# Kernel optimization log

Hardware: AMD Instinct MI355X
Metric: run time of the kernel (lower is better)

Reference implementation:

```python
import jax, jax.numpy as jnp
import numpy as np

# wav2vec2 feature-extractor conv stack config: (kernel, stride) per layer, 512 channels
CONV_CFG = [(10, 5), (3, 2), (3, 2), (3, 2), (3, 2), (2, 2), (2, 2)]
C = 512
PROJ = 256
HID = 128
NCLS = 5
N_WORDS = 64
B = 8
L = 40000


def _conv1d(h, w, stride):
    # h: [B, Cin, T], w: [Cout, Cin, K]
    return jax.lax.conv_general_dilated(
        h, w, window_strides=(stride,), padding='VALID',
        dimension_numbers=('NCH', 'OIH', 'NCH'))


def setup_inputs() -> dict:
    key = jax.random.key(0)
    ks = jax.random.split(key, 16)
    x = jax.random.normal(ks[0], (B, L), dtype=jnp.float32)
    word_ids = jax.random.randint(ks[1], (B,), 0, N_WORDS)
    convs = {}
    cin = 1
    for i, (k, s) in enumerate(CONV_CFG):
        fan = cin * k
        convs[f'conv{i}'] = jax.random.normal(ks[2 + i], (C, cin, k), dtype=jnp.float32) / np.sqrt(fan)
        cin = C
    gn_scale = jnp.ones((C,), dtype=jnp.float32)
    gn_bias = jnp.zeros((C,), dtype=jnp.float32)
    proj_w = jax.random.normal(ks[9], (PROJ, C), dtype=jnp.float32) / np.sqrt(C)
    proj_b = jnp.zeros((PROJ,), dtype=jnp.float32)
    cls_w1 = jax.random.normal(ks[10], (N_WORDS, PROJ, HID), dtype=jnp.float32) / np.sqrt(PROJ)
    cls_b1 = jnp.zeros((N_WORDS, HID), dtype=jnp.float32)
    cls_w2 = jax.random.normal(ks[11], (N_WORDS, HID, NCLS), dtype=jnp.float32) / np.sqrt(HID)
    cls_b2 = jnp.zeros((N_WORDS, NCLS), dtype=jnp.float32)
    return dict(x=x, word_ids=word_ids, gn_scale=gn_scale, gn_bias=gn_bias,
                proj_w=proj_w, proj_b=proj_b, cls_w1=cls_w1, cls_b1=cls_b1,
                cls_w2=cls_w2, cls_b2=cls_b2, **convs)


def _forward(x, convs, gn_scale, gn_bias, proj_w, proj_b, cls_w1, cls_b1, cls_w2, cls_b2, word_ids):
    h = x[:, None, :]  # [B,1,L]
    for i, (k, s) in enumerate(CONV_CFG):
        h = _conv1d(h, convs[i], s)
        if i == 0:
            # wav2vec2 group-norm: groups == channels -> per-channel norm over time
            mu = jnp.mean(h, axis=-1, keepdims=True)
            var = jnp.var(h, axis=-1, keepdims=True)
            h = (h - mu) * jax.lax.rsqrt(var + 1e-5)
            h = h * gn_scale[None, :, None] + gn_bias[None, :, None]
        h = jax.nn.gelu(h)
    feat = jnp.mean(h, axis=-1)                          # [B, 512] mean-pool over time
    feat = jax.nn.relu(feat @ proj_w.T + proj_b)         # [B, 256] (dropout = identity in eval)
    w1 = cls_w1[word_ids]                                # [B, 256, 128] routed gather
    h1 = jax.nn.relu(jnp.einsum('bd,bdh->bh', feat, w1) + cls_b1[word_ids])
    out = jnp.einsum('bh,bho->bo', h1, cls_w2[word_ids]) + cls_b2[word_ids]  # [B, 5]
    return out


def reference(x, word_ids, gn_scale, gn_bias, proj_w, proj_b, cls_w1, cls_b1, cls_w2, cls_b2,
              conv0, conv1, conv2, conv3, conv4, conv5, conv6):
    convs = [conv0, conv1, conv2, conv3, conv4, conv5, conv6]
    return _forward(x, convs, gn_scale, gn_bias, proj_w, proj_b,
                    cls_w1, cls_b1, cls_w2, cls_b2, word_ids)
```

## Files before the change

### kernel.cpp

```cpp
#include <hip/hip_runtime.h>
#include <hip/hip_bf16.h>

typedef unsigned short u16;
typedef short bf16x8 __attribute__((ext_vector_type(8)));
typedef float f32x4 __attribute__((ext_vector_type(4)));

#define CC 512

constexpr int vmimm(int n) {
    return (n & 0xF) | ((n >> 4) << 14) | (0x7 << 4) | (0xF << 8);
}

__device__ __forceinline__ float gelu_tanh(float x) {
    float x3 = x * x * x;
    float z  = 0.7978845608028654f * (x + 0.044715f * x3);
    float e  = __expf(2.0f * z);
    float th = 1.0f - 2.0f / (e + 1.0f);
    return 0.5f * x * (1.0f + th);
}

__device__ __forceinline__ u16 f2bf(float f) {
    union { float f; unsigned u; } v; v.f = f;
    unsigned r = v.u + 0x7fff + ((v.u >> 16) & 1);
    return (u16)(r >> 16);
}
__device__ __forceinline__ float bf2f(u16 h) {
    union { unsigned u; float f; } v; v.u = ((unsigned)h) << 16; return v.f;
}

__global__ __launch_bounds__(256) void conv0_stats(
    const float* __restrict__ x, const float* __restrict__ w0,
    float* __restrict__ part) {
    const int t0 = blockIdx.x * 64, b = blockIdx.y;
    __shared__ float xs[64 * 5 + 16];
    __shared__ float w0t[10 * 512];
    __shared__ float redS[4][512], redQ[4][512];
    for (int i = threadIdx.x; i < 64 * 5 + 5; i += 256) {
        int gi = t0 * 5 + i;
        xs[i] = (gi < 40000) ? x[b * 40000 + gi] : 0.0f;
    }
    for (int i = threadIdx.x; i < 5120; i += 256) {
        int c = i / 10, j = i - c * 10;
        w0t[j * 512 + c] = w0[i];
    }
    __syncthreads();
    const int lane = threadIdx.x & 63, wv = threadIdx.x >> 6;
    float wr[8][10];
#pragma unroll
    for (int q = 0; q < 8; ++q)
#pragma unroll
        for (int j = 0; j < 10; ++j) wr[q][j] = w0t[j * 512 + lane + 64 * q];
    float sacc[8] = {}, qacc[8] = {};
#pragma unroll
    for (int u = 0; u < 16; ++u) {
        const int tt = wv * 16 + u;
        const int t  = t0 + tt;
        float xv[10];
#pragma unroll
        for (int j = 0; j < 10; ++j) xv[j] = xs[tt * 5 + j];
#pragma unroll
        for (int q = 0; q < 8; ++q) {
            float a = 0.0f;
#pragma unroll
            for (int j = 0; j < 10; ++j) a = fmaf(wr[q][j], xv[j], a);
            if (t < 7999) {
                const float ar = bf2f(f2bf(a));
                sacc[q] += ar; qacc[q] += ar * ar;
            }
        }
    }
#pragma unroll
    for (int q = 0; q < 8; ++q) {
        redS[wv][lane + 64 * q] = sacc[q];
        redQ[wv][lane + 64 * q] = qacc[q];
    }
    __syncthreads();
    float* pp = part + (((size_t)blockIdx.x * 8 + b) * 512) * 2;
#pragma unroll
    for (int half = 0; half < 2; ++half) {
        const int c = half * 256 + threadIdx.x;
        const float s = redS[0][c] + redS[1][c] + redS[2][c] + redS[3][c];
        const float q = redQ[0][c] + redQ[1][c] + redQ[2][c] + redQ[3][c];
        pp[c * 2] = s; pp[c * 2 + 1] = q;
    }
}

__global__ __launch_bounds__(256) void stats_finalizeAB(
    const float* __restrict__ part, const float* __restrict__ gsc,
    const float* __restrict__ gbi, float* __restrict__ Af, float* __restrict__ Bf) {
    const int r4 = threadIdx.x & 63, kg = threadIdx.x >> 6;
    const int row = blockIdx.x * 64 + r4;
    float s = 0.0f, q = 0.0f;
    for (int k = kg; k < 125; k += 4) {
        const float2 v = *(const float2*)(part + ((size_t)k * 4096 + row) * 2);
        s += v.x; q += v.y;
    }
    __shared__ float rs[4][64], rq[4][64];
    rs[kg][r4] = s; rq[kg][r4] = q;
    __syncthreads();
    if (kg == 0) {
        s = rs[0][r4] + rs[1][r4] + rs[2][r4] + rs[3][r4];
        q = rq[0][r4] + rq[1][r4] + rq[2][r4] + rq[3][r4];
        float mean = s / 7999.0f;
        float var  = fmaxf(q / 7999.0f - mean * mean, 0.0f);
        float rstd = rsqrtf(var + 1e-5f);
        const int c = row & (CC - 1);
        float A = rstd * gsc[c];
        Af[row] = A;
        Bf[row] = gbi[c] - mean * A;
    }
}

__global__ __launch_bounds__(256) void conv0_norm(
    const float* __restrict__ x, const float* __restrict__ w0,
    const float* __restrict__ Af, const float* __restrict__ Bf,
    u16* __restrict__ actG) {
    const int t0 = blockIdx.x * 64, b = blockIdx.y;
    __shared__ float xs[64 * 5 + 16];
    __shared__ float w0t[10 * 512];
    for (int i = threadIdx.x; i < 64 * 5 + 5; i += 256) {
        int gi = t0 * 5 + i;
        xs[i] = (gi < 40000) ? x[b * 40000 + gi] : 0.0f;
    }
    for (int i = threadIdx.x; i < 5120; i += 256) {
        int c = i / 10, j = i - c * 10;
        w0t[j * 512 + c] = w0[i];
    }
    __syncthreads();
    const int lane = threadIdx.x & 63, wv = threadIdx.x >> 6;
    float wr[8][10];
    float Ar[8], Br[8];
#pragma unroll
    for (int q = 0; q < 8; ++q) {
        const int c = lane + 64 * q;
#pragma unroll
        for (int j = 0; j < 10; ++j) wr[q][j] = w0t[j * 512 + c];
        Ar[q] = Af[b * 512 + c];
        Br[q] = Bf[b * 512 + c];
    }
    u16* ob = actG + ((size_t)b * 8320 + t0 + wv * 16) * 512 + lane;
#pragma unroll
    for (int u = 0; u < 16; ++u) {
        const int tt = wv * 16 + u;
        const int t  = t0 + tt;
        float xv[10];
#pragma unroll
        for (int j = 0; j < 10; ++j) xv[j] = xs[tt * 5 + j];
#pragma unroll
        for (int q = 0; q < 8; ++q) {
            float a = 0.0f;
#pragma unroll
            for (int j = 0; j < 10; ++j) a = fmaf(wr[q][j], xv[j], a);
            u16 outv = 0;
            if (t < 7999) {
                const float ar = bf2f(f2bf(a));
                outv = f2bf(gelu_tanh(fmaf(ar, Ar[q], Br[q])));
            }
            ob[(size_t)u * 512 + 64 * q] = outv;
        }
    }
}

template <int K, int NL>
struct WtBatch { const float* src[NL]; u16* dst[NL]; };

template <int K, int NL>
__global__ __launch_bounds__(256) void wt_transform(WtBatch<K, NL> a) {
    constexpr int PLANE_U16 = K * 4096;
    const int cit = blockIdx.x, cob = blockIdx.y, l = blockIdx.z;
    const float* w = a.src[l];
    u16* dst = a.dst[l] + ((size_t)(cob * 16 + cit)) * PLANE_U16;
    for (int idx = threadIdx.x; idx < PLANE_U16; idx += 256) {
        const int r  = idx >> 9;
        const int cf = r / K, j = r - cf * K;
        const int li = (idx >> 3) & 63;
        const int e  = idx & 7;
        const int co = cob * 128 + cf * 16 + (li & 15);
        const int ci = cit * 32 + ((li >> 4) << 3) + e;
        dst[idx] = f2bf(w[((size_t)co * 512 + ci) * K + j]);
    }
}

template <int K, int TT>
__global__ __launch_bounds__(256, 2) void conv_mfma(
    const u16* __restrict__ act, int capIn,
    const u16* __restrict__ wt,
    u16* __restrict__ outAct, int capOut, int nTb) {
    constexpr int PLANE_B = K * 8192;
    constexpr int XH   = TT + 8;
    constexpr int TF   = TT / 32;
    constexpr int TXC  = XH * 8;
    constexpr int CPX  = TXC / 4;
    constexpr int NIX  = (CPX + 63) / 64;
    constexpr int XLAST = CPX - (NIX - 1) * 64;
    constexpr int CPW  = K * 128;
    constexpr int NIW  = K * 2;

    __shared__ __align__(16) u16 Xs[2][XH * 64];
    __shared__ __align__(16) u16 Ws[K * 4096];

    const int tid  = threadIdx.x;
    const int lane = tid & 63;
    const int wv   = tid >> 6;
    const int wco  = wv >> 1, wtt = wv & 1;
    const int l15  = lane & 15, l16 = lane >> 4;

    const int flat = blockIdx.x;
    const int xcd  = flat & 7, cob = (flat >> 3) & 3;
    const int G    = xcd + (flat >> 5) * 8;
    const int t_b  = G % nTb;
    const int b    = G / nTb;
    const int t0   = t_b * TT;
    const int x0   = t0 * 2;

    const char* abase = (const char*)(act + (size_t)b * capIn * 512);
    const char* wbase = (const char*)wt + (size_t)cob * (16 * PLANE_B);

    const char* xsA[NIX]; const char* xsB[NIX]; int xdst[NIX];
#pragma unroll
    for (int i = 0; i < NIX; ++i) {
        const int c  = wv * CPX + i * 64 + lane;
        const int xh = c >> 3;
        const int li = ((c & 7) * 16) ^ ((xh & 7) << 4);
        const int xx = min(x0 + 2 * xh + (li >> 6), capIn - 1);
        xsA[i] = abase + (size_t)xx * 1024 + (li & 63);
        xsB[i] = xsA[i] + 64;
        xdst[i] = (wv * CPX + i * 64) * 16;
    }
    const char* wsrc[NIW]; int wdst[NIW];
#pragma unroll
    for (int i = 0; i < NIW; ++i) {
        wsrc[i] = wbase + (size_t)(wv * CPW + i * 64 + lane) * 16;
        wdst[i] = (wv * CPW + i * 64) * 16;
    }

    auto stageX = [&](const char* (&xs)[NIX], u16* xb) {
#pragma unroll
        for (int i = 0; i < NIX; ++i)
            if (i < NIX - 1 || lane < XLAST)
                __builtin_amdgcn_global_load_lds(
                    (const __attribute__((address_space(1))) void*)xs[i],
                    (__attribute__((address_space(3))) void*)((char*)xb + xdst[i]),
                    16, 0, 0);
#pragma unroll
        for (int i = 0; i < NIX; ++i) xs[i] += 128;
    };
    auto stageW = [&]() {
#pragma unroll
        for (int i = 0; i < NIW; ++i)
            __builtin_amdgcn_global_load_lds(
                (const __attribute__((address_space(1))) void*)wsrc[i],
                (__attribute__((address_space(3))) void*)((char*)&Ws[0] + wdst[i]),
                16, 0, 0);
#pragma unroll
        for (int i = 0; i < NIW; ++i) wsrc[i] += PLANE_B;
    };

    int xoff[K][TF];
    int woff[K][4];
#pragma unroll
    for (int j = 0; j < K; ++j) {
#pragma unroll
        for (int tf = 0; tf < TF; ++tf) {
            const int tl = wtt * (TT / 2) + tf * 16 + l15;
            const int xl = 2 * tl + j;
            const int xh = xl >> 1, p = xl & 1;
            xoff[j][tf] = xh * 128 + ((p * 64 + l16 * 16) ^ ((xh & 7) << 4));
        }
#pragma unroll
        for (int cf = 0; cf < 4; ++cf)
            woff[j][cf] = (((wco * 4 + cf) * K + j) << 10) + lane * 16;
    }

    f32x4 acc[4][TF] = {};

    stageX(xsA, &Xs[0][0]);
    stageX(xsB, &Xs[1][0]);
    stageW();
    __syncthreads();

    auto body = [&](int cit, u16* xb, const char* (&xset)[NIX]) {
        bf16x8 xr[K][TF], wr[K][4];
#pragma unroll
        for (int j = 0; j < K; ++j) {
#pragma unroll
            for (int tf = 0; tf < TF; ++tf)
                xr[j][tf] = *(const bf16x8*)((const char*)xb + xoff[j][tf]);
#pragma unroll
            for (int cf = 0; cf < 4; ++cf)
                wr[j][cf] = *(const bf16x8*)((const char*)&Ws[0] + woff[j][cf]);
        }
        asm volatile("s_waitcnt lgkmcnt(0)" ::: "memory");
        __builtin_amdgcn_s_barrier();
        if (cit < 15) stageW();
        if (cit < 14) stageX(xset, xb);
#pragma unroll
        for (int j = 0; j < K; ++j)
#pragma unroll
            for (int cf = 0; cf < 4; ++cf)
#pragma unroll
                for (int tf = 0; tf < TF; ++tf)
                    acc[cf][tf] = __builtin_amdgcn_mfma_f32_16x16x32_bf16(
                        wr[j][cf], xr[j][tf], acc[cf][tf], 0, 0, 0);
        if (cit < 14) {
            __builtin_amdgcn_s_waitcnt(vmimm(NIX));
            __builtin_amdgcn_s_barrier();
        } else if (cit == 14) {
            __builtin_amdgcn_s_waitcnt(vmimm(0));
            __builtin_amdgcn_s_barrier();
        }
    };

#pragma unroll 1
    for (int c2 = 0; c2 < 16; c2 += 2) {
        body(c2,     &Xs[0][0], xsA);
        body(c2 + 1, &Xs[1][0], xsB);
    }

    u16* ob = outAct + (size_t)b * capOut * 512;
#pragma unroll
    for (int cf = 0; cf < 4; ++cf) {
#pragma unroll
        for (int tf = 0; tf < TF; ++tf) {
            const int tG  = t0 + wtt * (TT / 2) + tf * 16 + l15;
            const int coG = cob * 128 + wco * 64 + cf * 16 + l16 * 4;
            union { u16 s[4]; uint2 v; } pk;
#pragma unroll
            for (int r = 0; r < 4; ++r)
                pk.s[r] = f2bf(gelu_tanh(acc[cf][tf][r]));
            *(uint2*)(ob + (size_t)tG * 512 + coG) = pk.v;
        }
    }
}

__global__ __launch_bounds__(512) void feat_proj_kernel(
    const u16* __restrict__ act, int cap,
    const float* __restrict__ pw, const float* __restrict__ pb,
    float* __restrict__ pfeat) {
    const int b = blockIdx.x;
    __shared__ float fs[8][512];
    __shared__ float feat[CC];
    const int c8 = (threadIdx.x & 63) * 8;
    const int tg = threadIdx.x >> 6;
    float s[8] = {};
    for (int t = tg; t < 124; t += 8) {
        union { u16 u[8]; uint4 v; } in;
        in.v = *(const uint4*)(act + ((size_t)b * cap + t) * 512 + c8);
#pragma unroll
        for (int e = 0; e < 8; ++e) s[e] += bf2f(in.u[e]);
    }
#pragma unroll
    for (int e = 0; e < 8; ++e) fs[tg][c8 + e] = s[e];
    __syncthreads();
    {
        const int c = threadIdx.x;
        if (c < 512) {
            float acc = 0.0f;
#pragma unroll
            for (int g = 0; g < 8; ++g) acc += fs[g][c];
            feat[c] = acc * (1.0f / 124.0f);
        }
    }
    __syncthreads();
    if (threadIdx.x < 256) {
        const int j = threadIdx.x;
        const float* wr = pw + (size_t)j * CC;
        float acc = pb[j];
        for (int cc = 0; cc < CC; ++cc) acc = fmaf(feat[cc], wr[cc], acc);
        pfeat[b * 256 + j] = fmaxf(acc, 0.0f);
    }
}

__global__ __launch_bounds__(128) void cls_kernel(
    const float* __restrict__ pfeat, const int* __restrict__ wid,
    const float* __restrict__ w1, const float* __restrict__ b1,
    const float* __restrict__ w2, const float* __restrict__ b2,
    float* __restrict__ out) {
    const int b = blockIdx.x;
    const int id = wid[b];
    __shared__ float pf[256], h1[128];
    for (int d = threadIdx.x; d < 256; d += 128) pf[d] = pfeat[b * 256 + d];
    __syncthreads();
    {
        const int hh = threadIdx.x;
        const float* w1p = w1 + (size_t)id * 256 * 128;
        float s = b1[id * 128 + hh];
        for (int d = 0; d < 256; ++d) s = fmaf(pf[d], w1p[d * 128 + hh], s);
        h1[hh] = fmaxf(s, 0.0f);
    }
    __syncthreads();
    if (threadIdx.x < 5) {
        const float* w2p = w2 + (size_t)id * 128 * 5;
        float s = b2[id * 5 + threadIdx.x];
        for (int hh = 0; hh < 128; ++hh) s = fmaf(h1[hh], w2p[hh * 5 + threadIdx.x], s);
        out[b * 5 + threadIdx.x] = s;
    }
}

extern "C" void kernel_launch(void* const* d_in, const int* in_sizes, int n_in,
                              void* d_out, int out_size, void* d_ws, size_t ws_size,
                              hipStream_t stream) {
    const float* x   = (const float*)d_in[0];
    const int*   wid = (const int*)d_in[1];
    const float* gsc = (const float*)d_in[2];
    const float* gbi = (const float*)d_in[3];
    const float* pw  = (const float*)d_in[4];
    const float* pb  = (const float*)d_in[5];
    const float* w1  = (const float*)d_in[6];
    const float* b1  = (const float*)d_in[7];
    const float* w2  = (const float*)d_in[8];
    const float* b2  = (const float*)d_in[9];
    const float* cw[7];
    for (int i = 0; i < 7; ++i) cw[i] = (const float*)d_in[10 + i];

    char* ws = (char*)d_ws;
    const size_t SZ_ACTG = (size_t)8 * 8320 * 512 * 2;
    const size_t SZ_P    = (size_t)8 * 4224 * 512 * 2;
    const size_t SZ_Q    = (size_t)8 * 2176 * 512 * 2;
    u16* actG = (u16*)ws;
    u16* bufP = (u16*)(ws + SZ_ACTG);
    u16* bufQ = (u16*)(ws + SZ_ACTG + SZ_P);
    size_t off = SZ_ACTG + SZ_P + SZ_Q;
    u16* wtbuf[7];
    for (int i = 1; i <= 4; ++i) { wtbuf[i] = (u16*)(ws + off); off += (size_t)4 * 16 * (3 * 4096) * 2; }
    for (int i = 5; i <= 6; ++i) { wtbuf[i] = (u16*)(ws + off); off += (size_t)4 * 16 * (2 * 4096) * 2; }
    off = (off + 255) & ~(size_t)255;
    float* statsPart = (float*)(ws + off); off += (size_t)125 * 8 * 512 * 2 * 4;
    float* Af        = (float*)(ws + off); off += 4096 * 4;
    float* Bf        = (float*)(ws + off); off += 4096 * 4;
    float* pfeat     = (float*)(ws + off); off += 8 * 256 * 4;

    conv0_stats<<<dim3(125, 8), 256, 0, stream>>>(x, cw[0], statsPart);
    stats_finalizeAB<<<dim3(64), 256, 0, stream>>>(statsPart, gsc, gbi, Af, Bf);
    conv0_norm<<<dim3(125, 8), 256, 0, stream>>>(x, cw[0], Af, Bf, actG);

    {
        WtBatch<3, 4> a;
        for (int i = 0; i < 4; ++i) { a.src[i] = cw[1 + i]; a.dst[i] = wtbuf[1 + i]; }
        wt_transform<3, 4><<<dim3(16, 4, 4), 256, 0, stream>>>(a);
        WtBatch<2, 2> c;
        for (int i = 0; i < 2; ++i) { c.src[i] = cw[5 + i]; c.dst[i] = wtbuf[5 + i]; }
        wt_transform<2, 2><<<dim3(16, 4, 2), 256, 0, stream>>>(c);
    }

    conv_mfma<3, 96><<<dim3(42 * 32), 256, 0, stream>>>(actG, 8320, wtbuf[1], bufP, 4224, 42);
    conv_mfma<3, 96><<<dim3(21 * 32), 256, 0, stream>>>(bufP, 4224, wtbuf[2], bufQ, 2176, 21);
    conv_mfma<3, 64><<<dim3(16 * 32), 256, 0, stream>>>(bufQ, 2176, wtbuf[3], bufP, 4224, 16);
    conv_mfma<3, 64><<<dim3( 8 * 32), 256, 0, stream>>>(bufP, 4224, wtbuf[4], bufQ, 2176, 8);
    conv_mfma<2, 64><<<dim3( 4 * 32), 256, 0, stream>>>(bufQ, 2176, wtbuf[5], bufP, 4224, 4);
    conv_mfma<2, 64><<<dim3( 2 * 32), 256, 0, stream>>>(bufP, 4224, wtbuf[6], bufQ, 2176, 2);

    feat_proj_kernel<<<dim3(8), 512, 0, stream>>>(bufQ, 2176, pw, pb, pfeat);
    cls_kernel<<<dim3(8), 128, 0, stream>>>(pfeat, wid, w1, b1, w2, b2, (float*)d_out);
}
```

Measured before the change: 302.4 us.

## Double-buffer conv weight tiles and prefetch X and W one step ahead

```diff
diff --git a/kernel.cpp b/kernel.cpp
--- a/kernel.cpp
+++ b/kernel.cpp
@@ -197,7 +197,7 @@
     constexpr int NIW  = K * 2;
 
     __shared__ __align__(16) u16 Xs[2][XH * 64];
-    __shared__ __align__(16) u16 Ws[K * 4096];
+    __shared__ __align__(16) u16 Ws[2][K * 4096];
 
     const int tid  = threadIdx.x;
     const int lane = tid & 63;
@@ -216,15 +216,14 @@
     const char* abase = (const char*)(act + (size_t)b * capIn * 512);
     const char* wbase = (const char*)wt + (size_t)cob * (16 * PLANE_B);
 
-    const char* xsA[NIX]; const char* xsB[NIX]; int xdst[NIX];
+    const char* xsrc[NIX]; int xdst[NIX];
 #pragma unroll
     for (int i = 0; i < NIX; ++i) {
         const int c  = wv * CPX + i * 64 + lane;
         const int xh = c >> 3;
         const int li = ((c & 7) * 16) ^ ((xh & 7) << 4);
         const int xx = min(x0 + 2 * xh + (li >> 6), capIn - 1);
-        xsA[i] = abase + (size_t)xx * 1024 + (li & 63);
-        xsB[i] = xsA[i] + 64;
+        xsrc[i] = abase + (size_t)xx * 1024 + (li & 63);
         xdst[i] = (wv * CPX + i * 64) * 16;
     }
     const char* wsrc[NIW]; int wdst[NIW];
@@ -234,23 +233,23 @@
         wdst[i] = (wv * CPW + i * 64) * 16;
     }
 
-    auto stageX = [&](const char* (&xs)[NIX], u16* xb) {
+    auto stageX = [&](u16* xb) {
 #pragma unroll
         for (int i = 0; i < NIX; ++i)
             if (i < NIX - 1 || lane < XLAST)
                 __builtin_amdgcn_global_load_lds(
-                    (const __attribute__((address_space(1))) void*)xs[i],
+                    (const __attribute__((address_space(1))) void*)xsrc[i],
                     (__attribute__((address_space(3))) void*)((char*)xb + xdst[i]),
                     16, 0, 0);
 #pragma unroll
-        for (int i = 0; i < NIX; ++i) xs[i] += 128;
+        for (int i = 0; i < NIX; ++i) xsrc[i] += 64;
     };
-    auto stageW = [&]() {
+    auto stageW = [&](u16* wb) {
 #pragma unroll
         for (int i = 0; i < NIW; ++i)
             __builtin_amdgcn_global_load_lds(
                 (const __attribute__((address_space(1))) void*)wsrc[i],
-                (__attribute__((address_space(3))) void*)((char*)&Ws[0] + wdst[i]),
+                (__attribute__((address_space(3))) void*)((char*)wb + wdst[i]),
                 16, 0, 0);
 #pragma unroll
         for (int i = 0; i < NIW; ++i) wsrc[i] += PLANE_B;
@@ -274,26 +273,27 @@
 
     f32x4 acc[4][TF] = {};
 
-    stageX(xsA, &Xs[0][0]);
-    stageX(xsB, &Xs[1][0]);
-    stageW();
-    __syncthreads();
-
-    auto body = [&](int cit, u16* xb, const char* (&xset)[NIX]) {
+    stageX(&Xs[0][0]);
+    stageW(&Ws[0][0]);
+    __syncthreads();
+
+#pragma unroll 1
+    for (int cit = 0; cit < 16; ++cit) {
+        const int cur = cit & 1;
+        if (cit < 15) {
+            stageW(&Ws[cur ^ 1][0]);
+            stageX(&Xs[cur ^ 1][0]);
+        }
         bf16x8 xr[K][TF], wr[K][4];
 #pragma unroll
         for (int j = 0; j < K; ++j) {
 #pragma unroll
             for (int tf = 0; tf < TF; ++tf)
-                xr[j][tf] = *(const bf16x8*)((const char*)xb + xoff[j][tf]);
+                xr[j][tf] = *(const bf16x8*)((const char*)&Xs[cur][0] + xoff[j][tf]);
 #pragma unroll
             for (int cf = 0; cf < 4; ++cf)
-                wr[j][cf] = *(const bf16x8*)((const char*)&Ws[0] + woff[j][cf]);
-        }
-        asm volatile("s_waitcnt lgkmcnt(0)" ::: "memory");
-        __builtin_amdgcn_s_barrier();
-        if (cit < 15) stageW();
-        if (cit < 14) stageX(xset, xb);
+                wr[j][cf] = *(const bf16x8*)((const char*)&Ws[cur][0] + woff[j][cf]);
+        }
 #pragma unroll
         for (int j = 0; j < K; ++j)
 #pragma unroll
@@ -302,19 +302,10 @@
                 for (int tf = 0; tf < TF; ++tf)
                     acc[cf][tf] = __builtin_amdgcn_mfma_f32_16x16x32_bf16(
                         wr[j][cf], xr[j][tf], acc[cf][tf], 0, 0, 0);
-        if (cit < 14) {
-            __builtin_amdgcn_s_waitcnt(vmimm(NIX));
-            __builtin_amdgcn_s_barrier();
-        } else if (cit == 14) {
+        if (cit < 15) {
             __builtin_amdgcn_s_waitcnt(vmimm(0));
             __builtin_amdgcn_s_barrier();
         }
-    };
-
-#pragma unroll 1
-    for (int c2 = 0; c2 < 16; c2 += 2) {
-        body(c2,     &Xs[0][0], xsA);
-        body(c2 + 1, &Xs[1][0], xsB);
     }
 
     u16* ob = outAct + (size_t)b * capOut * 512;
```

Result: slower. 324.0 us (+7.2%).
